# Optimization experiments

Hardware: AMD Instinct MI355X
Metric: run time of the kernel (lower is better)

The kernel has to match this reference:

```python
import jax, jax.numpy as jnp
import numpy as np

DIM = 1536
NUM_HEADS = 16
HEAD_DIM = DIM // NUM_HEADS  # 96
ROPE_DIM = HEAD_DIM // 2     # 48
PT_SEQ = 32
FT_SEQ = 32
EPS = 1e-6


def _rope_tables():
    # VisionRotaryEmbedding(dim=48, pt_seq_len=32): 2D axial rotary tables
    f = 1.0 / (10000.0 ** (np.arange(0, ROPE_DIM, 2, dtype=np.float32)[: ROPE_DIM // 2] / ROPE_DIM))
    pos = np.arange(FT_SEQ, dtype=np.float32) / FT_SEQ * PT_SEQ
    freqs = pos[:, None] * f[None, :]                       # [32, 24]
    freqs = np.repeat(freqs, 2, axis=-1)                    # [32, 48] interleaved
    row = np.broadcast_to(freqs[:, None, :], (FT_SEQ, FT_SEQ, ROPE_DIM))
    col = np.broadcast_to(freqs[None, :, :], (FT_SEQ, FT_SEQ, ROPE_DIM))
    grid = np.concatenate([row, col], axis=-1).reshape(-1, HEAD_DIM)  # [1024, 96]
    return jnp.asarray(np.cos(grid)), jnp.asarray(np.sin(grid))


def _apply_rotary(x, cos, sin):
    # x: [B, S, H, D]; cos/sin: [S, D]; interleaved (use_real_unbind_dim=-1) rotation
    xr = x.reshape(*x.shape[:-1], -1, 2)
    x_rot = jnp.stack([-xr[..., 1], xr[..., 0]], axis=-1).reshape(x.shape)
    return x * cos[None, :, None, :] + x_rot * sin[None, :, None, :]


def _rms_norm(x, w):
    var = jnp.mean(jnp.square(x), axis=-1, keepdims=True)
    return x * jax.lax.rsqrt(var + EPS) * w


def setup_inputs() -> dict:
    key = jax.random.key(0)
    ks = jax.random.split(key, 12)
    s = 1.0 / np.sqrt(DIM)
    return {
        "hidden_states": jax.random.normal(ks[0], (8, 1024, DIM), dtype=jnp.float32),
        "Wq": jax.random.normal(ks[1], (DIM, DIM), dtype=jnp.float32) * s,
        "bq": jax.random.normal(ks[2], (DIM,), dtype=jnp.float32) * 0.01,
        "Wk": jax.random.normal(ks[3], (DIM, DIM), dtype=jnp.float32) * s,
        "bk": jax.random.normal(ks[4], (DIM,), dtype=jnp.float32) * 0.01,
        "Wv": jax.random.normal(ks[5], (DIM, DIM), dtype=jnp.float32) * s,
        "bv": jax.random.normal(ks[6], (DIM,), dtype=jnp.float32) * 0.01,
        "q_norm_w": jnp.ones((HEAD_DIM,), dtype=jnp.float32),
        "k_norm_w": jnp.ones((HEAD_DIM,), dtype=jnp.float32),
        "Wo": jax.random.normal(ks[7], (DIM, DIM), dtype=jnp.float32) * s,
        "bo": jax.random.normal(ks[8], (DIM,), dtype=jnp.float32) * 0.01,
    }


def reference(hidden_states, Wq, bq, Wk, bk, Wv, bv, q_norm_w, k_norm_w, Wo, bo):
    B, S, _ = hidden_states.shape
    cos, sin = _rope_tables()  # [S, HEAD_DIM], constants

    q = hidden_states @ Wq.T + bq
    k = hidden_states @ Wk.T + bk
    v = hidden_states @ Wv.T + bv
    q = q.reshape(B, S, NUM_HEADS, HEAD_DIM)
    k = k.reshape(B, S, NUM_HEADS, HEAD_DIM)
    v = v.reshape(B, S, NUM_HEADS, HEAD_DIM)

    q = _rms_norm(q, q_norm_w)
    k = _rms_norm(k, k_norm_w)
    q = _apply_rotary(q, cos, sin)
    k = _apply_rotary(k, cos, sin)

    scale = 1.0 / np.sqrt(HEAD_DIM)
    scores = jnp.einsum("bshd,bthd->bhst", q, k) * scale  # [B, H, S, S]
    probs = jax.nn.softmax(scores, axis=-1)
    out = jnp.einsum("bhst,bthd->bshd", probs, v)          # [B, S, H, D]
    out = out.reshape(B, S, DIM)
    return out @ Wo.T + bo
```

## Files before the change

kernel.cpp:

```cpp
#include <hip/hip_runtime.h>
#include <hip/hip_bf16.h>
#include <math.h>

typedef __hip_bfloat16 bf16;
typedef __attribute__((ext_vector_type(8))) short short8;
typedef __attribute__((ext_vector_type(4))) short short4v;
typedef __attribute__((ext_vector_type(4))) float f32x4;

#define MFMA16(a, b, c) __builtin_amdgcn_mfma_f32_16x16x32_bf16((a), (b), (c), 0, 0, 0)

typedef const __attribute__((address_space(1))) void GVOID;
typedef __attribute__((address_space(3))) void LVOID;

__device__ __forceinline__ float b2f(short s) {
    union { unsigned u; float f; } v;
    v.u = ((unsigned)(unsigned short)s) << 16;
    return v.f;
}
__device__ __forceinline__ short f2b(float f) {
    union { float f; unsigned u; } v;
    v.f = f;
    unsigned r = v.u + 0x7fffu + ((v.u >> 16) & 1u);
    return (short)(r >> 16);
}
__device__ __forceinline__ unsigned packbf2(float a, float b) {
    float2 t; t.x = a; t.y = b;
    __hip_bfloat162 h = __float22bfloat162_rn(t);
    union { __hip_bfloat162 h; unsigned u; } cv; cv.h = h;
    return cv.u;
}
__device__ __forceinline__ short bf2s(float x) {
    __hip_bfloat16 h = __float2bfloat16(x);
    union { __hip_bfloat16 h; short s; } cv; cv.h = h;
    return cv.s;
}

__global__ __launch_bounds__(256) void prep_kernel(
    const unsigned* __restrict__ X,
    const void* __restrict__ bq, const void* __restrict__ bk,
    const void* __restrict__ bv, const void* __restrict__ bo,
    const void* __restrict__ qw, const void* __restrict__ kw,
    int* __restrict__ flag, float* __restrict__ biasqkv, float* __restrict__ boc,
    float* __restrict__ qwc, float* __restrict__ kwc,
    float* __restrict__ cosT, float* __restrict__ sinT)
{
    const int tid = threadIdx.x;
    if (blockIdx.x == 0) {
        __shared__ int cnt;
        if (tid == 0) cnt = 0;
        __syncthreads();
        unsigned w = X[tid];
        unsigned e = (w >> 7) & 0xFFu;
        if (e > 140u) atomicAdd(&cnt, 1);
        __syncthreads();
        const int f = (cnt >= 16) ? 1 : 0;
        if (tid == 0) *flag = f;
        for (int i = tid; i < 6336; i += 256) {
            const void* src; float* dst; int j;
            if (i < 4608) {
                int m = i / 1536; j = i - m * 1536;
                src = (m == 0) ? bq : (m == 1) ? bk : bv; dst = biasqkv + i;
            } else if (i < 6144) { j = i - 4608; src = bo; dst = boc + j; }
            else if (i < 6240)   { j = i - 6144; src = qw; dst = qwc + j; }
            else                 { j = i - 6240; src = kw; dst = kwc + j; }
            *dst = f ? ((const float*)src)[j] : b2f(((const short*)src)[j]);
        }
    } else {
        int idx = (blockIdx.x - 1) * 256 + tid;
        if (idx >= 1024 * 96) return;
        int p = idx / 96;
        int d = idx - p * 96;
        int r = p >> 5, c = p & 31;
        int inRow = (d < 48);
        int dd = inRow ? d : d - 48;
        float pos = inRow ? (float)r : (float)c;
        float ex = -(float)(dd & ~1) / 48.0f;
        float f = powf(10000.0f, ex);
        float ang = pos * f;
        cosT[idx] = cosf(ang);
        sinT[idx] = sinf(ang);
    }
}

__device__ __forceinline__ void canon8(const void* src, short* dst, int i, int f) {
    short8 o;
    if (f) {
        const float* s = (const float*)src + (size_t)i * 8;
#pragma unroll
        for (int j = 0; j < 8; ++j) o[j] = f2b(s[j]);
    } else {
        o = ((const short8*)src)[i];
    }
    ((short8*)dst)[i] = o;
}

__global__ __launch_bounds__(256) void canon_all_kernel(
    const void* __restrict__ X,
    const void* __restrict__ s0, const void* __restrict__ s1,
    const void* __restrict__ s2, const void* __restrict__ s3,
    short* __restrict__ dX,
    short* __restrict__ d0, short* __restrict__ d1,
    short* __restrict__ d2, short* __restrict__ d3,
    const int* __restrict__ flag)
{
    const int f = *flag;
    const int bid = blockIdx.x;
    if (bid < 6144) {
        canon8(X, dX, bid * 256 + threadIdx.x, f);
    } else {
        const int wb = bid - 6144;
        const int m = wb / 1152;
        const int i = (wb - m * 1152) * 256 + threadIdx.x;
        const void* src = (m == 0) ? s0 : (m == 1) ? s1 : (m == 2) ? s2 : s3;
        short* dst = (m == 0) ? d0 : (m == 1) ? d1 : (m == 2) ? d2 : d3;
        canon8(src, dst, i, f);
    }
}

__global__ __launch_bounds__(256) void gemm128_kernel(
    const bf16* __restrict__ A, const bf16* __restrict__ Bw,
    const float* __restrict__ bias,
    bf16* __restrict__ O0, bf16* __restrict__ O1, bf16* __restrict__ O2,
    int K, const int* __restrict__ outFlag)
{
    __shared__ __align__(16) short As[2][128 * 64];
    __shared__ __align__(16) short Bs[2][128 * 64];

    const int tid = threadIdx.x;
    const int lane = tid & 63, w = tid >> 6;
    const int wr = w >> 1, wc = w & 1;
    const int li = lane & 15, lg = lane >> 4;

    const int total = gridDim.x * gridDim.y;
    const int pp = blockIdx.y * gridDim.x + blockIdx.x;
    const int lb = (pp & 7) * (total >> 3) + (pp >> 3);
    const int nb = lb % gridDim.x;
    const int mb = lb / gridDim.x;
    const long mBase = (long)mb * 128;
    const long nGlob = (long)nb * 128;

    const bf16* aSrc[4]; const bf16* bSrc[4]; int ldsOff[4];
#pragma unroll
    for (int u = 0; u < 4; ++u) {
        const int L = u * 4096 + tid * 16;
        const int S = L ^ (((L >> 7) & 7) << 4);
        const int srow = S >> 7;
        const int scol = (S & 127) >> 1;
        aSrc[u] = A + (mBase + srow) * K + scol;
        bSrc[u] = Bw + (nGlob + srow) * K + scol;
        ldsOff[u] = L >> 1;
    }
    const int rxor = (li & 7) << 4;
    int kidx[2];
#pragma unroll
    for (int ks = 0; ks < 2; ++ks)
        kidx[ks] = ((ks * 64 + lg * 16) ^ rxor) >> 1;

    f32x4 acc[4][4] = {};
    const int NT = K >> 6;

    auto stage = [&](int tt, int bb) {
        const long kc = (long)tt * 64;
#pragma unroll
        for (int u = 0; u < 4; ++u)
            __builtin_amdgcn_global_load_lds((GVOID*)(aSrc[u] + kc),
                                             (LVOID*)&As[bb][ldsOff[u]], 16, 0, 0);
#pragma unroll
        for (int u = 0; u < 4; ++u)
            __builtin_amdgcn_global_load_lds((GVOID*)(bSrc[u] + kc),
                                             (LVOID*)&Bs[bb][ldsOff[u]], 16, 0, 0);
    };

    stage(0, 0);
    asm volatile("s_waitcnt vmcnt(0)" ::: "memory");
    __builtin_amdgcn_s_barrier();
    asm volatile("" ::: "memory");

    for (int t = 0; t < NT; ++t) {
        const int cb = t & 1;
        if (t + 1 < NT) stage(t + 1, cb ^ 1);
        const short* Ab = &As[cb][0];
        const short* Bb = &Bs[cb][0];
#pragma unroll
        for (int ks = 0; ks < 2; ++ks) {
            short8 fa[4], fb[4];
#pragma unroll
            for (int m = 0; m < 4; ++m)
                fa[m] = *(const short8*)(Ab + (wr * 64 + m * 16 + li) * 64 + kidx[ks]);
#pragma unroll
            for (int n = 0; n < 4; ++n)
                fb[n] = *(const short8*)(Bb + (wc * 64 + n * 16 + li) * 64 + kidx[ks]);
            __builtin_amdgcn_sched_barrier(0);
            __builtin_amdgcn_s_setprio(1);
#pragma unroll
            for (int m = 0; m < 4; ++m)
#pragma unroll
                for (int n = 0; n < 4; ++n)
                    acc[m][n] = MFMA16(fa[m], fb[n], acc[m][n]);
            __builtin_amdgcn_s_setprio(0);
            __builtin_amdgcn_sched_barrier(0);
        }
        asm volatile("s_waitcnt vmcnt(0)" ::: "memory");
        __builtin_amdgcn_s_barrier();
        asm volatile("" ::: "memory");
    }

    const int f32out = outFlag ? *outFlag : 0;
    const int mat = nb / 12;
    const long colBase = nGlob - (long)mat * 1536;
    bf16* Ob = (mat == 0) ? O0 : (mat == 1) ? O1 : O2;
    if (f32out) {
        float* Cf = (float*)Ob;
#pragma unroll
        for (int n = 0; n < 4; ++n) {
            const long col = colBase + wc * 64 + n * 16 + li;
            const float bv = bias[nGlob + wc * 64 + n * 16 + li];
#pragma unroll
            for (int m = 0; m < 4; ++m) {
                const long row = mBase + wr * 64 + m * 16 + lg * 4;
#pragma unroll
                for (int i = 0; i < 4; ++i)
                    Cf[(row + i) * 1536 + col] = acc[m][n][i] + bv;
            }
        }
    } else {
#pragma unroll
        for (int n = 0; n < 4; ++n) {
            const long col = colBase + wc * 64 + n * 16 + li;
            const float bv = bias[nGlob + wc * 64 + n * 16 + li];
#pragma unroll
            for (int m = 0; m < 4; ++m) {
                const long row = mBase + wr * 64 + m * 16 + lg * 4;
#pragma unroll
                for (int i = 0; i < 4; ++i)
                    Ob[(row + i) * 1536 + col] = __float2bfloat16(acc[m][n][i] + bv);
            }
        }
    }
}

__global__ __launch_bounds__(256) void norm_rope2_kernel(
    bf16* __restrict__ Qb, bf16* __restrict__ Kb,
    const float* __restrict__ qwc, const float* __restrict__ kwc,
    const float* __restrict__ cosT, const float* __restrict__ sinT,
    float qscale)
{
    bf16* T = blockIdx.y ? Kb : Qb;
    const float* wgt = blockIdx.y ? kwc : qwc;
    const float scale = blockIdx.y ? 1.0f : qscale;

    const int row = blockIdx.x * 256 + threadIdx.x;
    const int tok = row >> 4;
    const int h = row & 15;
    const int spos = tok & 1023;
    bf16* p = T + (size_t)tok * 1536 + h * 96;

    float x[96];
#pragma unroll
    for (int v = 0; v < 12; ++v) {
        short8 t = *(const short8*)(p + v * 8);
#pragma unroll
        for (int j = 0; j < 8; ++j) x[v * 8 + j] = b2f(t[j]);
    }
    float ss = 0.f;
#pragma unroll
    for (int d = 0; d < 96; ++d) ss += x[d] * x[d];
    const float rn = scale / sqrtf(ss * (1.0f / 96.0f) + 1e-6f);

    const float* cr = cosT + spos * 96;
    const float* sr = sinT + spos * 96;

#pragma unroll
    for (int v = 0; v < 12; ++v) {
        short8 o;
#pragma unroll
        for (int j = 0; j < 8; j += 2) {
            const int d = v * 8 + j;
            const float x0 = x[d] * rn * wgt[d];
            const float x1 = x[d + 1] * rn * wgt[d + 1];
            o[j]     = f2b(x0 * cr[d] - x1 * sr[d]);
            o[j + 1] = f2b(x1 * cr[d + 1] + x0 * sr[d + 1]);
        }
        *(short8*)(p + v * 8) = o;
    }
}

__global__ __launch_bounds__(512, 2) void attn_kernel(
    const bf16* __restrict__ Q, const bf16* __restrict__ K,
    const bf16* __restrict__ V, bf16* __restrict__ O)
{
    __shared__ __align__(16) short Ks[64 * 96];
    __shared__ __align__(16) short Vt[96 * 64];
    __shared__ __align__(16) short Pl[8][16 * 64];

    const int tid = threadIdx.x;
    const int l = tid & 63, w = tid >> 6;
    const int li = l & 15, lg = l >> 4;

    const int p = blockIdx.x;
    const int lb = (p & 7) * 128 + (p >> 3);
    const int qt = lb & 7;
    const int bh = lb >> 3;
    const int b = bh >> 4, h = bh & 15;
    const size_t tokBase = (size_t)b * 1024;

    short8 aq[3];
    {
        const bf16* qp = Q + (tokBase + qt * 128 + w * 16 + li) * 1536 + h * 96;
#pragma unroll
        for (int kk = 0; kk < 3; ++kk)
            aq[kk] = *(const short8*)(qp + kk * 32 + lg * 8);
    }

    float m_r = -1e30f, l_r = 0.f;
    f32x4 o[6] = {};

    const bool kst = (w >= 4);
    int kr[3], km[3], kso[3];
#pragma unroll
    for (int u = 0; u < 3; ++u) {
        const int c = (tid - 256) + 256 * u;
        const int crr = c / 12;
        kr[u] = crr;
        km[u] = (c - crr * 12) * 8;
        kso[u] = (crr * 96 + km[u]) ^ ((crr & 7) << 3);
    }
    const int t2 = tid >> 3;
    const int dh = tid & 7;
    const bf16* vbase = V + (tokBase + 2 * t2) * 1536 + h * 96 + dh * 12;
    short* Plw = &Pl[w][0];

    const int kswz = (li & 7) << 3;
    const int vswz = ((li >> 1) & 7) << 3;

    short8 kreg[3];
    short4v vr0[3], vr1[3];
    if (kst) {
#pragma unroll
        for (int u = 0; u < 3; ++u)
            kreg[u] = *(const short8*)(K + (tokBase + kr[u]) * 1536 + h * 96 + km[u]);
    } else {
#pragma unroll
        for (int u = 0; u < 3; ++u) {
            vr0[u] = *(const short4v*)(vbase + u * 4);
            vr1[u] = *(const short4v*)(vbase + 1536 + u * 4);
        }
    }

    for (int t0 = 0; t0 < 1024; t0 += 64) {
        __syncthreads();
        if (kst) {
#pragma unroll
            for (int u = 0; u < 3; ++u)
                *(short8*)&Ks[kso[u]] = kreg[u];
        } else {
            unsigned* Vt32 = (unsigned*)Vt;
#pragma unroll
            for (int u = 0; u < 3; ++u)
#pragma unroll
                for (int j = 0; j < 4; ++j) {
                    const int d = dh * 12 + u * 4 + j;
                    const unsigned pk = ((unsigned)(unsigned short)vr0[u][j]) |
                                        (((unsigned)(unsigned short)vr1[u][j]) << 16);
                    Vt32[(d * 32 + t2) ^ (((d >> 1) & 7) << 2)] = pk;
                }
        }
        __syncthreads();

        const int t1 = (t0 + 64 < 1024) ? t0 + 64 : t0;
        if (kst) {
#pragma unroll
            for (int u = 0; u < 3; ++u)
                kreg[u] = *(const short8*)(K + (tokBase + t1 + kr[u]) * 1536 + h * 96 + km[u]);
        } else {
            const bf16* vp = vbase + (size_t)t1 * 1536;
#pragma unroll
            for (int u = 0; u < 3; ++u) {
                vr0[u] = *(const short4v*)(vp + u * 4);
                vr1[u] = *(const short4v*)(vp + 1536 + u * 4);
            }
        }

        f32x4 s4[4] = {};
#pragma unroll
        for (int kk = 0; kk < 3; ++kk) {
#pragma unroll
            for (int kn = 0; kn < 4; ++kn) {
                short8 fk = *(const short8*)&Ks[((kn * 16 + li) * 96 + kk * 32 + lg * 8) ^ kswz];
                s4[kn] = MFMA16(fk, aq[kk], s4[kn]);
            }
        }

        {
            float mk[4];
#pragma unroll
            for (int kn = 0; kn < 4; ++kn)
                mk[kn] = fmaxf(fmaxf(s4[kn][0], s4[kn][1]),
                               fmaxf(s4[kn][2], s4[kn][3]));
            float pm = fmaxf(fmaxf(mk[0], mk[1]), fmaxf(mk[2], mk[3]));
            pm = fmaxf(pm, __shfl_xor(pm, 16));
            pm = fmaxf(pm, __shfl_xor(pm, 32));

            float alpha = 1.0f;
            const bool need = (pm > m_r + 8.0f);
            if (need) { alpha = exp2f(m_r - pm); m_r = pm; }
            const float mn = m_r;

            float rs = 0.f;
            unsigned long long pq[4];
#pragma unroll
            for (int kn = 0; kn < 4; ++kn) {
                float p0 = exp2f(s4[kn][0] - mn);
                float p1 = exp2f(s4[kn][1] - mn);
                float p2 = exp2f(s4[kn][2] - mn);
                float p3 = exp2f(s4[kn][3] - mn);
                rs += (p0 + p1) + (p2 + p3);
                pq[kn] = ((unsigned long long)packbf2(p0, p1)) |
                         (((unsigned long long)packbf2(p2, p3)) << 32);
            }
            rs += __shfl_xor(rs, 16);
            rs += __shfl_xor(rs, 32);
            l_r = l_r * alpha + rs;
            if (need) {
#pragma unroll
                for (int dn = 0; dn < 6; ++dn)
#pragma unroll
                    for (int i = 0; i < 4; ++i) o[dn][i] *= alpha;
            }
            const int rowS = li * 64;
#pragma unroll
            for (int kn = 0; kn < 4; ++kn)
                *(unsigned long long*)&Plw[(rowS + kn * 16 + lg * 4) ^ kswz] = pq[kn];
        }

#pragma unroll
        for (int kt = 0; kt < 2; ++kt) {
            short8 pa = *(const short8*)&Plw[(li * 64 + kt * 32 + lg * 8) ^ kswz];
#pragma unroll
            for (int dn = 0; dn < 6; ++dn) {
                short8 fv = *(const short8*)&Vt[((dn * 16 + li) * 64 + kt * 32 + lg * 8) ^ vswz];
                o[dn] = MFMA16(fv, pa, o[dn]);
            }
        }
    }

    {
        const float inv = 1.0f / l_r;
        const size_t row = tokBase + qt * 128 + w * 16 + li;
#pragma unroll
        for (int dn = 0; dn < 6; ++dn) {
            short4v ov;
#pragma unroll
            for (int i = 0; i < 4; ++i) ov[i] = bf2s(o[dn][i] * inv);
            *(short4v*)&O[row * 1536 + h * 96 + dn * 16 + lg * 4] = ov;
        }
    }
}

extern "C" void kernel_launch(void* const* d_in, const int* in_sizes, int n_in,
                              void* d_out, int out_size, void* d_ws, size_t ws_size,
                              hipStream_t stream) {
    const void* X  = d_in[0];
    const void* Wq = d_in[1];
    const void* bq = d_in[2];
    const void* Wk = d_in[3];
    const void* bk = d_in[4];
    const void* Wv = d_in[5];
    const void* bv = d_in[6];
    const void* qw = d_in[7];
    const void* kw = d_in[8];
    const void* Wo = d_in[9];
    const void* bo = d_in[10];

    char* ws = (char*)d_ws;
    size_t off = 0;
    int* flag = (int*)ws;                      off += 256;
    float* cosT = (float*)(ws + off);          off += 1024 * 96 * 4;
    float* sinT = (float*)(ws + off);          off += 1024 * 96 * 4;
    float* biasqkv = (float*)(ws + off);       off += 4608 * 4;
    float* boc  = (float*)(ws + off);          off += 1536 * 4;
    float* qwc  = (float*)(ws + off);          off += 128 * 4;
    float* kwc  = (float*)(ws + off);          off += 128 * 4;
    off = (off + 255) & ~(size_t)255;
    bf16* Wc  = (bf16*)(ws + off);             off += (size_t)4608 * 1536 * 2;
    bf16* Woc = (bf16*)(ws + off);             off += (size_t)1536 * 1536 * 2;
    bf16* Xc  = (bf16*)(ws + off);             off += (size_t)8192 * 1536 * 2;
    bf16* Qb  = (bf16*)(ws + off);             off += (size_t)8192 * 1536 * 2;
    bf16* Kb  = (bf16*)(ws + off);             off += (size_t)8192 * 1536 * 2;
    bf16* Vb  = (bf16*)(ws + off);             off += (size_t)8192 * 1536 * 2;
    bf16* AO  = Xc;

    prep_kernel<<<385, 256, 0, stream>>>((const unsigned*)X, bq, bk, bv, bo, qw, kw,
                                         flag, biasqkv, boc, qwc, kwc, cosT, sinT);

    canon_all_kernel<<<10752, 256, 0, stream>>>(
        X, Wq, Wk, Wv, Wo,
        (short*)Xc, (short*)Wc, (short*)(Wc + (size_t)1536 * 1536),
        (short*)(Wc + (size_t)2 * 1536 * 1536), (short*)Woc, flag);

    gemm128_kernel<<<dim3(36, 64), 256, 0, stream>>>(
        Xc, Wc, biasqkv, Qb, Kb, Vb, 1536, nullptr);

    const float qscale = (float)(0.10206207261596577 * 1.4426950408889634);
    norm_rope2_kernel<<<dim3(512, 2), 256, 0, stream>>>(Qb, Kb, qwc, kwc, cosT, sinT, qscale);

    attn_kernel<<<1024, 512, 0, stream>>>(Qb, Kb, Vb, AO);

    gemm128_kernel<<<dim3(12, 64), 256, 0, stream>>>(
        AO, Woc, boc, (bf16*)d_out, (bf16*)d_out, (bf16*)d_out, 1536, flag);
}
```

Measured before the change: 392.3 us.

## Double-buffer K/V tiles in attention and use permlane32 swap for reductions

```diff
diff --git a/kernel.cpp b/kernel.cpp
--- a/kernel.cpp
+++ b/kernel.cpp
@@ -6,6 +6,7 @@
 typedef __attribute__((ext_vector_type(8))) short short8;
 typedef __attribute__((ext_vector_type(4))) short short4v;
 typedef __attribute__((ext_vector_type(4))) float f32x4;
+typedef __attribute__((ext_vector_type(2))) int int2v;
 
 #define MFMA16(a, b, c) __builtin_amdgcn_mfma_f32_16x16x32_bf16((a), (b), (c), 0, 0, 0)
 
@@ -34,6 +35,24 @@
     union { __hip_bfloat16 h; short s; } cv; cv.h = h;
     return cv.s;
 }
+
+#if __has_builtin(__builtin_amdgcn_permlane32_swap)
+__device__ __forceinline__ float addx32(float x) {
+    union { float f; int i; } c; c.f = x;
+    int2v r = __builtin_amdgcn_permlane32_swap(c.i, c.i, false, false);
+    union { int i; float f; } a, b; a.i = r[0]; b.i = r[1];
+    return a.f + b.f;
+}
+__device__ __forceinline__ float maxx32(float x) {
+    union { float f; int i; } c; c.f = x;
+    int2v r = __builtin_amdgcn_permlane32_swap(c.i, c.i, false, false);
+    union { int i; float f; } a, b; a.i = r[0]; b.i = r[1];
+    return fmaxf(a.f, b.f);
+}
+#else
+__device__ __forceinline__ float addx32(float x) { return x + __shfl_xor(x, 32); }
+__device__ __forceinline__ float maxx32(float x) { return fmaxf(x, __shfl_xor(x, 32)); }
+#endif
 
 __global__ __launch_bounds__(256) void prep_kernel(
     const unsigned* __restrict__ X,
@@ -289,8 +308,8 @@
     const bf16* __restrict__ Q, const bf16* __restrict__ K,
     const bf16* __restrict__ V, bf16* __restrict__ O)
 {
-    __shared__ __align__(16) short Ks[64 * 96];
-    __shared__ __align__(16) short Vt[96 * 64];
+    __shared__ __align__(16) short Ks[2][64 * 96];
+    __shared__ __align__(16) short Vt[2][96 * 64];
     __shared__ __align__(16) short Pl[8][16 * 64];
 
     const int tid = threadIdx.x;
@@ -335,26 +354,27 @@
 
     short8 kreg[3];
     short4v vr0[3], vr1[3];
-    if (kst) {
-#pragma unroll
-        for (int u = 0; u < 3; ++u)
-            kreg[u] = *(const short8*)(K + (tokBase + kr[u]) * 1536 + h * 96 + km[u]);
-    } else {
-#pragma unroll
-        for (int u = 0; u < 3; ++u) {
-            vr0[u] = *(const short4v*)(vbase + u * 4);
-            vr1[u] = *(const short4v*)(vbase + 1536 + u * 4);
-        }
-    }
-
-    for (int t0 = 0; t0 < 1024; t0 += 64) {
-        __syncthreads();
+    auto loadT = [&](int tt) {
         if (kst) {
 #pragma unroll
             for (int u = 0; u < 3; ++u)
-                *(short8*)&Ks[kso[u]] = kreg[u];
+                kreg[u] = *(const short8*)(K + (tokBase + tt + kr[u]) * 1536 + h * 96 + km[u]);
         } else {
-            unsigned* Vt32 = (unsigned*)Vt;
+            const bf16* vp = vbase + (size_t)tt * 1536;
+#pragma unroll
+            for (int u = 0; u < 3; ++u) {
+                vr0[u] = *(const short4v*)(vp + u * 4);
+                vr1[u] = *(const short4v*)(vp + 1536 + u * 4);
+            }
+        }
+    };
+    auto writeT = [&](int bb) {
+        if (kst) {
+#pragma unroll
+            for (int u = 0; u < 3; ++u)
+                *(short8*)&Ks[bb][kso[u]] = kreg[u];
+        } else {
+            unsigned* Vt32 = (unsigned*)&Vt[bb][0];
 #pragma unroll
             for (int u = 0; u < 3; ++u)
 #pragma unroll
@@ -365,31 +385,28 @@
                     Vt32[(d * 32 + t2) ^ (((d >> 1) & 7) << 2)] = pk;
                 }
         }
-        __syncthreads();
-
-        const int t1 = (t0 + 64 < 1024) ? t0 + 64 : t0;
-        if (kst) {
-#pragma unroll
-            for (int u = 0; u < 3; ++u)
-                kreg[u] = *(const short8*)(K + (tokBase + t1 + kr[u]) * 1536 + h * 96 + km[u]);
-        } else {
-            const bf16* vp = vbase + (size_t)t1 * 1536;
-#pragma unroll
-            for (int u = 0; u < 3; ++u) {
-                vr0[u] = *(const short4v*)(vp + u * 4);
-                vr1[u] = *(const short4v*)(vp + 1536 + u * 4);
-            }
-        }
+    };
+
+    loadT(0);
+    writeT(0);
+    loadT(64);
+    __syncthreads();
+
+    for (int t = 0; t < 16; ++t) {
+        const int cb = t & 1;
 
         f32x4 s4[4] = {};
 #pragma unroll
         for (int kk = 0; kk < 3; ++kk) {
 #pragma unroll
             for (int kn = 0; kn < 4; ++kn) {
-                short8 fk = *(const short8*)&Ks[((kn * 16 + li) * 96 + kk * 32 + lg * 8) ^ kswz];
+                short8 fk = *(const short8*)&Ks[cb][((kn * 16 + li) * 96 + kk * 32 + lg * 8) ^ kswz];
                 s4[kn] = MFMA16(fk, aq[kk], s4[kn]);
             }
         }
+
+        if (t < 15) writeT(cb ^ 1);
+        if (t < 14) loadT((t + 2) * 64);
 
         {
             float mk[4];
@@ -399,7 +416,7 @@
                                fmaxf(s4[kn][2], s4[kn][3]));
             float pm = fmaxf(fmaxf(mk[0], mk[1]), fmaxf(mk[2], mk[3]));
             pm = fmaxf(pm, __shfl_xor(pm, 16));
-            pm = fmaxf(pm, __shfl_xor(pm, 32));
+            pm = maxx32(pm);
 
             float alpha = 1.0f;
             const bool need = (pm > m_r + 8.0f);
@@ -419,7 +436,7 @@
                          (((unsigned long long)packbf2(p2, p3)) << 32);
             }
             rs += __shfl_xor(rs, 16);
-            rs += __shfl_xor(rs, 32);
+            rs = addx32(rs);
             l_r = l_r * alpha + rs;
             if (need) {
 #pragma unroll
@@ -438,10 +455,12 @@
             short8 pa = *(const short8*)&Plw[(li * 64 + kt * 32 + lg * 8) ^ kswz];
 #pragma unroll
             for (int dn = 0; dn < 6; ++dn) {
-                short8 fv = *(const short8*)&Vt[((dn * 16 + li) * 64 + kt * 32 + lg * 8) ^ vswz];
+                short8 fv = *(const short8*)&Vt[cb][((dn * 16 + li) * 64 + kt * 32 + lg * 8) ^ vswz];
                 o[dn] = MFMA16(fv, pa, o[dn]);
             }
         }
+
+        __syncthreads();
     }
 
     {
```

Result: faster. 382.4 us (median of 2 runs) (-2.5%).
